# Kernel optimization log

Measured on AMD Instinct MI355X. Metric: run time of the kernel, lower is better.

## Reference

```python
import jax, jax.numpy as jnp
import numpy as np

N_CAND = 21  # tf.linspace(0, 1, 21) candidate pool
SOFTMIN_TEMP = 100.0


def _tree_constants(max_depth: int):
    """Signed split->descendant matrix M (S,N) and node->parent one-hot P (N,N)."""
    n_splits = 2 ** max_depth - 1
    n_nodes = 2 ** (max_depth + 1) - 1
    M = np.zeros((n_splits, n_nodes), np.float32)
    for s in range(n_splits):
        for n in range(n_nodes):
            a = n
            while a > 0:
                p = (a - 1) // 2
                if p == s:
                    # left-subtree descendants get -1, right-subtree +1
                    M[s, n] = -1.0 if a == 2 * s + 1 else 1.0
                    break
                a = p
    P = np.zeros((n_nodes, n_nodes), np.float32)
    for i in range(1, n_nodes):
        P[i, (i - 1) // 2] = 1.0
    return jnp.asarray(M), jnp.asarray(P), n_splits, n_nodes


def setup_inputs() -> dict:
    key = jax.random.key(0)
    kx, kw, kb = jax.random.split(key, 3)
    B, F = 512, 512
    max_depth = 8
    n_splits = 2 ** max_depth - 1
    x = jax.random.normal(kx, (B, F), dtype=jnp.float32)
    # VarianceScaling(scale=2.0, mode='fan_in') ~ std sqrt(2/F)
    W = jax.random.normal(kw, (F, n_splits), dtype=jnp.float32) * np.sqrt(2.0 / F).astype(np.float32)
    # keras RandomNormal default stddev=0.05
    b = jax.random.normal(kb, (n_splits,), dtype=jnp.float32) * 0.05
    return {"x": x, "W": W, "b": b, "max_depth": max_depth}


def reference(x, W, b, max_depth):
    M, P, n_splits, n_nodes = _tree_constants(int(max_depth))
    # q per split, then min over ancestor splits (method 0)
    q_split = x @ W + b                                   # (B, S)
    q_bsn = q_split[:, :, None] * M[None] + 1.0 - jnp.abs(M)[None]  # (B, S, N)
    q_node = jnp.min(q_bsn, axis=1)                       # (B, N)

    a_cand = jnp.linspace(0.0, 1.0, N_CAND)               # (C,)
    qn = q_node[:, :, None]                               # (B, N, 1)
    sqr = jnp.where(a_cand <= qn + 0.5, (a_cand - (qn + 0.5)) ** 2, 0.0)
    # reg part sums over the size-1 leading axis of a -> just a^2 (reg_lambda=1.0 in call)
    g_a = 0.5 * a_cand ** 2 + 0.5 * jnp.sum(sqr, axis=0)  # (N, C)

    eye = jnp.eye(n_nodes, dtype=jnp.float32)

    def body(carry, _):
        n2g, _ = carry
        g_grp = n2g.T @ g_a                               # (N, C): group-summed objective
        w = jax.nn.softmax(-SOFTMIN_TEMP * g_grp, axis=1)
        a_grp = jnp.sum(a_cand * w, axis=1)               # (N,) soft argmin over candidates
        a_node = n2g @ a_grp                              # (N,) broadcast group value to nodes
        a_par = (P @ a_node)[1:]
        a_par = jnp.concatenate([jnp.ones((1,), a_node.dtype), a_par])
        viol = a_node - a_par
        t = jnp.argmax(viol)
        cond = (jnp.max(viol) <= 1e-8) & (t > 0)
        t_oh = jax.nn.one_hot(t, n_nodes, dtype=jnp.float32)
        p_oh = t_oh @ P
        n2g = n2g + jnp.where(cond, 1.0, 0.0) * jnp.outer(t_oh, p_oh - t_oh)
        return (n2g, a_node), None

    (_, a_node), _ = jax.lax.scan(body, (eye, jnp.zeros(n_nodes, jnp.float32)), None,
                                  length=n_nodes + 1)
    trajectory = jnp.clip(q_node, 0.0, a_node[None, :])   # (B, N)
    return trajectory
```

## Files before the change

### kernel.cpp

```cpp
#include <hip/hip_runtime.h>
#include <hip/hip_bf16.h>
#include <math.h>

#define BATCH 512
#define FDIM  512
#define NSPL  255
#define NNOD  511
#define NC    21


__global__ __launch_bounds__(256) void k_qgemm(const float* __restrict__ x,
                                               const float* __restrict__ W,
                                               float* __restrict__ partial,
                                               int fpc) {
  __shared__ float Ws[64 * 68];
  __shared__ float xT[64 * 68];
  const int tid = threadIdx.x;
  const int s0 = blockIdx.x * 64;
  const int b0 = blockIdx.y * 64;
  const int f0 = blockIdx.z * fpc;
  const int sx = tid & 15;
  const int by = tid >> 4;
  float acc[4][4];
#pragma unroll
  for (int i = 0; i < 4; ++i)
#pragma unroll
    for (int j = 0; j < 4; ++j) acc[i][j] = 0.f;

  for (int fc = f0; fc < f0 + fpc; fc += 64) {
    {
      int si = tid & 63, fr = tid >> 6;
#pragma unroll
      for (int r = 0; r < 16; ++r) {
        int fi = fr + r * 4;
        int s = s0 + si;
        Ws[fi * 68 + si] = (s < NSPL) ? W[(fc + fi) * NSPL + s] : 0.f;
      }
      int j = tid & 63, ir = tid >> 6;
#pragma unroll
      for (int r = 0; r < 16; ++r) {
        int i = ir + r * 4;
        xT[j * 68 + i] = x[(b0 + i) * FDIM + (fc + j)];
      }
    }
    __syncthreads();
#pragma unroll 8
    for (int f = 0; f < 64; ++f) {
      float4 av = *(const float4*)&Ws[f * 68 + sx * 4];
      float4 xv = *(const float4*)&xT[f * 68 + by * 4];
      const float a4[4] = {av.x, av.y, av.z, av.w};
      const float x4[4] = {xv.x, xv.y, xv.z, xv.w};
#pragma unroll
      for (int i = 0; i < 4; ++i)
#pragma unroll
        for (int j = 0; j < 4; ++j) acc[i][j] += a4[i] * x4[j];
    }
    __syncthreads();
  }

  float* pout = partial + (size_t)blockIdx.z * (256 * BATCH);
#pragma unroll
  for (int i = 0; i < 4; ++i) {
    int s = s0 + sx * 4 + i;
    if (s < NSPL) {
      float4 v = make_float4(acc[i][0], acc[i][1], acc[i][2], acc[i][3]);
      *(float4*)&pout[s * BATCH + b0 + by * 4] = v;
    }
  }
}

__global__ __launch_bounds__(256) void k_qreduce(const float* __restrict__ partial,
                                                 const float* __restrict__ bias,
                                                 float* __restrict__ qsT, int n) {
  int idx = blockIdx.x * 256 + threadIdx.x;
  if (idx >= NSPL * BATCH) return;
  int s = idx >> 9;
  float v = 0.f;
  for (int c = 0; c < n; ++c) v += partial[(size_t)c * (256 * BATCH) + idx];
  qsT[idx] = v + bias[s];
}

__global__ __launch_bounds__(256) void k_qsplitT_fb(const float* __restrict__ x,
                                                    const float* __restrict__ W,
                                                    const float* __restrict__ bias,
                                                    float* __restrict__ qsT) {
  const int s = threadIdx.x;
  const int b0 = blockIdx.x * 8;
  if (s >= NSPL) return;
  float acc0[8], acc1[8];
#pragma unroll
  for (int i = 0; i < 8; ++i) { acc0[i] = 0.f; acc1[i] = 0.f; }
#pragma unroll 2
  for (int f = 0; f < 256; ++f) {
    float w0 = W[f * NSPL + s];
    float w1 = W[(f + 256) * NSPL + s];
#pragma unroll
    for (int i = 0; i < 8; ++i) {
      acc0[i] += x[(b0 + i) * FDIM + f] * w0;
      acc1[i] += x[(b0 + i) * FDIM + f + 256] * w1;
    }
  }
  float bs = bias[s];
#pragma unroll
  for (int i = 0; i < 8; ++i) qsT[s * BATCH + b0 + i] = (acc0[i] + acc1[i]) + bs;
}

__device__ __forceinline__ float qnode_walk(const float* __restrict__ qsT, int n, int b) {
  float q = 1.0f;
  int a = n;
  while (a > 0) {
    int p = (a - 1) >> 1;
    float v = qsT[p * BATCH + b];
    q = fminf(q, (a & 1) ? -v : v);
    a = p;
  }
  return q;
}

__global__ __launch_bounds__(256) void k_ga(const float* __restrict__ qsT,
                                            float* __restrict__ ga,
                                            double* __restrict__ agrp0) {
  const int n = blockIdx.x;
  const int tid = threadIdx.x;
  __shared__ float qs[BATCH];
  __shared__ double part[4][NC];
  __shared__ float gaRow[NC];
#pragma unroll
  for (int rep = 0; rep < 2; ++rep) {
    int b = tid + rep * 256;
    qs[b] = qnode_walk(qsT, n, b);
  }
  __syncthreads();
  if (tid < 4 * NC) {
    int c = tid % NC, chunk = tid / NC;
    double ac = 0.05 * (double)c;
    double ssum = 0.0;
    int b0 = chunk * 128;
    for (int b = b0; b < b0 + 128; ++b) {
      float qh = qs[b] + 0.5f;
      double dqh = (double)qh;
      if (ac <= dqh) { double d = ac - dqh; ssum += d * d; }
    }
    part[chunk][c] = ssum;
  }
  __syncthreads();
  if (tid < NC) {
    double ac = 0.05 * (double)tid;
    double ssum = ((part[0][tid] + part[1][tid]) + part[2][tid]) + part[3][tid];
    float gv = (float)(0.5 * ac * ac + 0.5 * ssum);
    ga[n * NC + tid] = gv;
    gaRow[tid] = gv;
  }
  __syncthreads();
  if (tid == 0) {
    double z[NC], m = -1e300;
#pragma unroll
    for (int c = 0; c < NC; ++c) { z[c] = -100.0 * (double)gaRow[c]; m = fmax(m, z[c]); }
    double S = 0.0;
#pragma unroll
    for (int c = 0; c < NC; ++c) { z[c] = exp(z[c] - m); S += z[c]; }
    double A = 0.0;
#pragma unroll
    for (int c = 0; c < NC; ++c) A += (0.05 * (double)c) * (z[c] / S);
    agrp0[n] = A;
  }
}

__global__ __launch_bounds__(64) void k_scan(const float* __restrict__ ga_g,
                                             const double* __restrict__ agrp0,
                                             double* __restrict__ a_node_out) {
  __shared__ float gaS[NNOD * NC];
  __shared__ double agrp[512];
  __shared__ double anode[512];
  __shared__ float kfS[512];
  const int lane = threadIdx.x;

  {
    const float4* src = (const float4*)ga_g;
    float4* dst = (float4*)gaS;
    const int n4 = (NNOD * NC) / 4;
#pragma unroll 4
    for (int i = lane; i < n4; i += 64) dst[i] = src[i];
    if (lane < (NNOD * NC) - n4 * 4) gaS[n4 * 4 + lane] = ga_g[n4 * 4 + lane];
  }
  for (int i = lane; i < 512; i += 64) {
    agrp[i] = (i < NNOD) ? agrp0[i] : 0.0;
    anode[i] = 0.0;
    kfS[i] = 0.0f;
  }
  __syncthreads();

  int t = 0, p = 0;
  double areg[8];
  int iter = 0;
  for (;;) {
    if (iter > 0) {
      int j = lane >> 5, c = lane & 31;
      int g = j ? p : t;
      double z = -1e300;
      if (c < NC) {
        double acc = (1.0 - (double)kfS[g]) * (double)gaS[g * NC + c];
        int l = 2 * g + 1, r = 2 * g + 2;
        if (l < NNOD) acc = acc + (double)kfS[l] * (double)gaS[l * NC + c];
        if (r < NNOD) acc = acc + (double)kfS[r] * (double)gaS[r * NC + c];
        z = -100.0 * acc;
      }
      double m = z;
#pragma unroll
      for (int off = 16; off >= 1; off >>= 1) m = fmax(m, __shfl_xor(m, off, 32));
      double e = (c < NC) ? exp(z - m) : 0.0;
      double S = e;
#pragma unroll
      for (int off = 16; off >= 1; off >>= 1) S += __shfl_xor(S, off, 32);
      double term = (c < NC) ? (0.05 * (double)c) * (e / S) : 0.0;
#pragma unroll
      for (int off = 16; off >= 1; off >>= 1) term += __shfl_xor(term, off, 32);
      if (c == 0) agrp[g] = term;
      __syncthreads();
    }

#pragma unroll
    for (int u = 0; u < 8; ++u) {
      int n = lane + (u << 6);
      if (n < NNOD) {
        double kn = (double)kfS[n];
        double agn = agrp[n];
        double an;
        if (n == 0) an = agn;
        else an = kn * agrp[(n - 1) >> 1] + (1.0 - kn) * agn;
        areg[u] = an;
        anode[n] = an;
      }
    }
    __syncthreads();

    double bv = -1e300; int bi = 0x7fffffff;
#pragma unroll
    for (int u = 0; u < 8; ++u) {
      int n = lane + (u << 6);
      if (n < NNOD) {
        double ap = (n == 0) ? 1.0 : anode[(n - 1) >> 1];
        double vi = areg[u] - ap;
        if (vi > bv) { bv = vi; bi = n; }
      }
    }
#pragma unroll
    for (int off = 32; off >= 1; off >>= 1) {
      double ov = __shfl_xor(bv, off, 64);
      int oi = __shfl_xor(bi, off, 64);
      if (ov > bv || (ov == bv && oi < bi)) { bv = ov; bi = oi; }
    }

    bool cond = (bv <= 1e-8) && (bi > 0);
    if (!cond || iter == 511) break;
    t = bi; p = (t - 1) >> 1;
    if (lane == 0) kfS[t] += 1.0f;
    __syncthreads();
    ++iter;
  }

#pragma unroll
  for (int u = 0; u < 8; ++u) {
    int n = lane + (u << 6);
    if (n < NNOD) a_node_out[n] = areg[u];
  }
}

__global__ __launch_bounds__(256) void k_out(const float* __restrict__ qsT,
                                             const double* __restrict__ a_node,
                                             float* __restrict__ out) {
  __shared__ float col[NSPL];
  const int b = blockIdx.x;
  const int tid = threadIdx.x;
  if (tid < NSPL) col[tid] = qsT[tid * BATCH + b];
  __syncthreads();
#pragma unroll
  for (int rep = 0; rep < 2; ++rep) {
    int n = tid + rep * 256;
    if (n < NNOD) {
      float q = 1.0f;
      int a = n;
      while (a > 0) {
        int p = (a - 1) >> 1;
        float v = col[p];
        q = fminf(q, (a & 1) ? -v : v);
        a = p;
      }
      double r = fmin(fmax((double)q, 0.0), a_node[n]);
      out[(size_t)b * NNOD + n] = (float)r;
    }
  }
}

extern "C" void kernel_launch(void* const* d_in, const int* in_sizes, int n_in,
                              void* d_out, int out_size, void* d_ws, size_t ws_size,
                              hipStream_t stream) {
  (void)in_sizes; (void)n_in; (void)out_size;
  const float* x    = (const float*)d_in[0];
  const float* W    = (const float*)d_in[1];
  const float* bias = (const float*)d_in[2];
  float* out = (float*)d_out;

  char* ws = (char*)d_ws;
  const size_t PART_STRIDE = 256 * BATCH * sizeof(float);
  const size_t TAIL = 575488;

  int n = 8;
  while (n > 1 && (size_t)n * PART_STRIDE + TAIL > ws_size) n >>= 1;
  bool splitk_ok = ((size_t)n * PART_STRIDE + TAIL <= ws_size);

  size_t P = splitk_ok ? (size_t)n * PART_STRIDE : 0;
  float*  qsT    = (float*) (ws + P);
  float*  ga     = (float*) (ws + P + 524288);
  double* agrp0  = (double*)(ws + P + 567296);
  double* a_node = (double*)(ws + P + 571392);

  if (splitk_ok) {
    float* partial = (float*)ws;
    k_qgemm<<<dim3(4, 8, n), dim3(256), 0, stream>>>(x, W, partial, 512 / n);
    k_qreduce<<<dim3(510), dim3(256), 0, stream>>>(partial, bias, qsT, n);
  } else {
    k_qsplitT_fb<<<dim3(64), dim3(256), 0, stream>>>(x, W, bias, qsT);
  }
  k_ga<<<dim3(NNOD), dim3(256), 0, stream>>>(qsT, ga, agrp0);
  k_scan<<<dim3(1), dim3(64), 0, stream>>>(ga, agrp0, a_node);
  k_out<<<dim3(BATCH), dim3(256), 0, stream>>>(qsT, a_node, out);
}
```

Measured before the change: 92.86 us.

## Fuse all stages into one persistent kernel with hierarchical grid barriers

Merges the split-K GEMM, reduction, per-node objective, serial scan and output kernels into a single 512-block kernel separated by atomic grid barriers, removing four launch gaps. While block 0 runs the serial scan, the other blocks precompute their q_node values so that after the last barrier they only clamp and store. A memset of the barrier area is added per call, and the design depends on all 512 blocks being co-resident (two per CU via launch bounds), otherwise it deadlocks.

```diff
diff --git a/kernel.cpp b/kernel.cpp
--- a/kernel.cpp
+++ b/kernel.cpp
@@ -9,75 +9,334 @@
 #define NC    21
 
 
-__global__ __launch_bounds__(256) void k_qgemm(const float* __restrict__ x,
-                                               const float* __restrict__ W,
-                                               float* __restrict__ partial,
-                                               int fpc) {
-  __shared__ float Ws[64 * 68];
-  __shared__ float xT[64 * 68];
+__device__ __forceinline__ unsigned* bslot(unsigned* bar, int i) { return bar + (size_t)i * 32; }
+
+__device__ __forceinline__ void grid_bar(unsigned* bar, int k, int bid, int tid) {
+  __syncthreads();
+  if (tid == 0) {
+    __threadfence();
+    unsigned cell = (unsigned)(bid & 7);
+    unsigned v = __hip_atomic_fetch_add(bslot(bar, 1 + k * 8 + (int)cell), 1u,
+                                        __ATOMIC_ACQ_REL, __HIP_MEMORY_SCOPE_AGENT);
+    if (v == 63u) {
+      unsigned r = __hip_atomic_fetch_add(bslot(bar, 33 + k), 1u,
+                                          __ATOMIC_ACQ_REL, __HIP_MEMORY_SCOPE_AGENT);
+      if (r == 7u)
+        __hip_atomic_store(bslot(bar, 37 + k), 1u, __ATOMIC_RELEASE, __HIP_MEMORY_SCOPE_AGENT);
+    }
+    while (__hip_atomic_load(bslot(bar, 37 + k), __ATOMIC_ACQUIRE, __HIP_MEMORY_SCOPE_AGENT) != 1u)
+      __builtin_amdgcn_s_sleep(2);
+    __threadfence();
+  }
+  __syncthreads();
+}
+
+__device__ __forceinline__ float qnode_walk(const float* __restrict__ qsT, int n, int b) {
+  float q = 1.0f;
+  int a = n;
+  while (a > 0) {
+    int p = (a - 1) >> 1;
+    float v = qsT[p * BATCH + b];
+    q = fminf(q, (a & 1) ? -v : v);
+    a = p;
+  }
+  return q;
+}
+
+__global__ __launch_bounds__(256, 2) void k_mega(
+    const float* __restrict__ x, const float* __restrict__ W,
+    const float* __restrict__ bias,
+    float* __restrict__ partial, float* __restrict__ qsT,
+    float* __restrict__ ga, double* __restrict__ agrp0,
+    double* __restrict__ a_node, float* __restrict__ out,
+    unsigned* __restrict__ bar, int fpc, int nchunks) {
+  __shared__ __align__(16) char smraw[53168];
   const int tid = threadIdx.x;
-  const int s0 = blockIdx.x * 64;
-  const int b0 = blockIdx.y * 64;
-  const int f0 = blockIdx.z * fpc;
-  const int sx = tid & 15;
-  const int by = tid >> 4;
-  float acc[4][4];
-#pragma unroll
-  for (int i = 0; i < 4; ++i)
-#pragma unroll
-    for (int j = 0; j < 4; ++j) acc[i][j] = 0.f;
-
-  for (int fc = f0; fc < f0 + fpc; fc += 64) {
+  const int bid = blockIdx.x;
+
+  if (bid < 32 * nchunks) {
+    float* Ws = (float*)smraw;
+    float* xT = Ws + 64 * 68;
+    const int s0 = (bid & 3) * 64;
+    const int b0 = ((bid >> 2) & 7) * 64;
+    const int bz = bid >> 5;
+    const int f0 = bz * fpc;
+    const int sx = tid & 15;
+    const int by = tid >> 4;
+    float acc[4][4];
+#pragma unroll
+    for (int i = 0; i < 4; ++i)
+#pragma unroll
+      for (int j = 0; j < 4; ++j) acc[i][j] = 0.f;
+
+    for (int fc = f0; fc < f0 + fpc; fc += 64) {
+      {
+        int si = tid & 63, fr = tid >> 6;
+#pragma unroll
+        for (int r = 0; r < 16; ++r) {
+          int fi = fr + r * 4;
+          int s = s0 + si;
+          Ws[fi * 68 + si] = (s < NSPL) ? W[(fc + fi) * NSPL + s] : 0.f;
+        }
+        int j = tid & 63, ir = tid >> 6;
+#pragma unroll
+        for (int r = 0; r < 16; ++r) {
+          int i = ir + r * 4;
+          xT[j * 68 + i] = x[(b0 + i) * FDIM + (fc + j)];
+        }
+      }
+      __syncthreads();
+#pragma unroll 8
+      for (int f = 0; f < 64; ++f) {
+        float4 av = *(const float4*)&Ws[f * 68 + sx * 4];
+        float4 xv = *(const float4*)&xT[f * 68 + by * 4];
+        const float a4[4] = {av.x, av.y, av.z, av.w};
+        const float x4[4] = {xv.x, xv.y, xv.z, xv.w};
+#pragma unroll
+        for (int i = 0; i < 4; ++i)
+#pragma unroll
+          for (int j = 0; j < 4; ++j) acc[i][j] += a4[i] * x4[j];
+      }
+      __syncthreads();
+    }
+
+    float* pout = partial + (size_t)bz * (256 * BATCH);
+#pragma unroll
+    for (int i = 0; i < 4; ++i) {
+      int s = s0 + sx * 4 + i;
+      if (s < NSPL) {
+        float4 v = make_float4(acc[i][0], acc[i][1], acc[i][2], acc[i][3]);
+        *(float4*)&pout[s * BATCH + b0 + by * 4] = v;
+      }
+    }
+  }
+  grid_bar(bar, 0, bid, tid);
+
+  if (bid < 510) {
+    int idx = bid * 256 + tid;
+    if (idx < NSPL * BATCH) {
+      int s = idx >> 9;
+      float v = 0.f;
+      for (int c = 0; c < nchunks; ++c) v += partial[(size_t)c * (256 * BATCH) + idx];
+      qsT[idx] = v + bias[s];
+    }
+  }
+  grid_bar(bar, 1, bid, tid);
+
+  if (bid < NNOD) {
+    const int n = bid;
+    float* qs = (float*)smraw;
+    double (*part)[NC] = (double (*)[NC])(smraw + 2048);
+    float* gaRow = (float*)(smraw + 2720);
+#pragma unroll
+    for (int rep = 0; rep < 2; ++rep) {
+      int b = tid + rep * 256;
+      qs[b] = qnode_walk(qsT, n, b);
+    }
+    __syncthreads();
+    if (tid < 4 * NC) {
+      int c = tid % NC, chunk = tid / NC;
+      double ac = 0.05 * (double)c;
+      double ssum = 0.0;
+      int b0 = chunk * 128;
+      for (int b = b0; b < b0 + 128; ++b) {
+        float qh = qs[b] + 0.5f;
+        double dqh = (double)qh;
+        if (ac <= dqh) { double d = ac - dqh; ssum += d * d; }
+      }
+      part[chunk][c] = ssum;
+    }
+    __syncthreads();
+    if (tid < NC) {
+      double ac = 0.05 * (double)tid;
+      double ssum = ((part[0][tid] + part[1][tid]) + part[2][tid]) + part[3][tid];
+      float gv = (float)(0.5 * ac * ac + 0.5 * ssum);
+      ga[n * NC + tid] = gv;
+      gaRow[tid] = gv;
+    }
+    __syncthreads();
+    if (tid == 0) {
+      double z[NC], m = -1e300;
+#pragma unroll
+      for (int c = 0; c < NC; ++c) { z[c] = -100.0 * (double)gaRow[c]; m = fmax(m, z[c]); }
+      double S = 0.0;
+#pragma unroll
+      for (int c = 0; c < NC; ++c) { z[c] = exp(z[c] - m); S += z[c]; }
+      double A = 0.0;
+#pragma unroll
+      for (int c = 0; c < NC; ++c) A += (0.05 * (double)c) * (z[c] / S);
+      agrp0[n] = A;
+    }
+  }
+  grid_bar(bar, 2, bid, tid);
+
+  float q0 = 0.f, q1 = 0.f;
+  if (bid == 0) {
+    if (tid < 64) {
+      float* gaS = (float*)smraw;
+      double* agrp = (double*)(smraw + 42928);
+      double* anode = (double*)(smraw + 47024);
+      float* kfS = (float*)(smraw + 51120);
+      const int lane = tid;
+      {
+        const float4* src = (const float4*)ga;
+        float4* dst = (float4*)gaS;
+        const int n4 = (NNOD * NC) / 4;
+#pragma unroll 4
+        for (int i = lane; i < n4; i += 64) dst[i] = src[i];
+        if (lane < (NNOD * NC) - n4 * 4) gaS[n4 * 4 + lane] = ga[n4 * 4 + lane];
+      }
+      for (int i = lane; i < 512; i += 64) {
+        agrp[i] = (i < NNOD) ? agrp0[i] : 0.0;
+        anode[i] = 0.0;
+        kfS[i] = 0.0f;
+      }
+      __threadfence_block();
+
+      int t = 0, p = 0;
+      double areg[8];
+      int iter = 0;
+      for (;;) {
+        if (iter > 0) {
+          int j = lane >> 5, c = lane & 31;
+          int g = j ? p : t;
+          double z = -1e300;
+          if (c < NC) {
+            double acc = (1.0 - (double)kfS[g]) * (double)gaS[g * NC + c];
+            int l = 2 * g + 1, r = 2 * g + 2;
+            if (l < NNOD) acc = acc + (double)kfS[l] * (double)gaS[l * NC + c];
+            if (r < NNOD) acc = acc + (double)kfS[r] * (double)gaS[r * NC + c];
+            z = -100.0 * acc;
+          }
+          double m = z;
+#pragma unroll
+          for (int off = 16; off >= 1; off >>= 1) m = fmax(m, __shfl_xor(m, off, 32));
+          double e = (c < NC) ? exp(z - m) : 0.0;
+          double S = e;
+#pragma unroll
+          for (int off = 16; off >= 1; off >>= 1) S += __shfl_xor(S, off, 32);
+          double term = (c < NC) ? (0.05 * (double)c) * (e / S) : 0.0;
+#pragma unroll
+          for (int off = 16; off >= 1; off >>= 1) term += __shfl_xor(term, off, 32);
+          if (c == 0) agrp[g] = term;
+          __threadfence_block();
+        }
+
+#pragma unroll
+        for (int u = 0; u < 8; ++u) {
+          int n = lane + (u << 6);
+          if (n < NNOD) {
+            double kn = (double)kfS[n];
+            double agn = agrp[n];
+            double an;
+            if (n == 0) an = agn;
+            else an = kn * agrp[(n - 1) >> 1] + (1.0 - kn) * agn;
+            areg[u] = an;
+            anode[n] = an;
+          }
+        }
+        __threadfence_block();
+
+        double bv = -1e300; int bi = 0x7fffffff;
+#pragma unroll
+        for (int u = 0; u < 8; ++u) {
+          int n = lane + (u << 6);
+          if (n < NNOD) {
+            double ap = (n == 0) ? 1.0 : anode[(n - 1) >> 1];
+            double vi = areg[u] - ap;
+            if (vi > bv) { bv = vi; bi = n; }
+          }
+        }
+#pragma unroll
+        for (int off = 32; off >= 1; off >>= 1) {
+          double ov = __shfl_xor(bv, off, 64);
+          int oi = __shfl_xor(bi, off, 64);
+          if (ov > bv || (ov == bv && oi < bi)) { bv = ov; bi = oi; }
+        }
+
+        bool cond = (bv <= 1e-8) && (bi > 0);
+        if (!cond || iter == 511) break;
+        t = bi; p = (t - 1) >> 1;
+        if (lane == 0) kfS[t] += 1.0f;
+        __threadfence_block();
+        ++iter;
+      }
+
+#pragma unroll
+      for (int u = 0; u < 8; ++u) {
+        int n = lane + (u << 6);
+        if (n < NNOD) a_node[n] = areg[u];
+      }
+    }
+  } else {
+    const int b = bid;
+    float* col = (float*)smraw;
+    if (tid < NSPL) col[tid] = qsT[tid * BATCH + b];
+    __syncthreads();
     {
-      int si = tid & 63, fr = tid >> 6;
-#pragma unroll
-      for (int r = 0; r < 16; ++r) {
-        int fi = fr + r * 4;
-        int s = s0 + si;
-        Ws[fi * 68 + si] = (s < NSPL) ? W[(fc + fi) * NSPL + s] : 0.f;
-      }
-      int j = tid & 63, ir = tid >> 6;
-#pragma unroll
-      for (int r = 0; r < 16; ++r) {
-        int i = ir + r * 4;
-        xT[j * 68 + i] = x[(b0 + i) * FDIM + (fc + j)];
-      }
-    }
-    __syncthreads();
-#pragma unroll 8
-    for (int f = 0; f < 64; ++f) {
-      float4 av = *(const float4*)&Ws[f * 68 + sx * 4];
-      float4 xv = *(const float4*)&xT[f * 68 + by * 4];
-      const float a4[4] = {av.x, av.y, av.z, av.w};
-      const float x4[4] = {xv.x, xv.y, xv.z, xv.w};
-#pragma unroll
-      for (int i = 0; i < 4; ++i)
-#pragma unroll
-        for (int j = 0; j < 4; ++j) acc[i][j] += a4[i] * x4[j];
-    }
-    __syncthreads();
-  }
-
-  float* pout = partial + (size_t)blockIdx.z * (256 * BATCH);
-#pragma unroll
-  for (int i = 0; i < 4; ++i) {
-    int s = s0 + sx * 4 + i;
-    if (s < NSPL) {
-      float4 v = make_float4(acc[i][0], acc[i][1], acc[i][2], acc[i][3]);
-      *(float4*)&pout[s * BATCH + b0 + by * 4] = v;
-    }
-  }
-}
-
-__global__ __launch_bounds__(256) void k_qreduce(const float* __restrict__ partial,
-                                                 const float* __restrict__ bias,
-                                                 float* __restrict__ qsT, int n) {
-  int idx = blockIdx.x * 256 + threadIdx.x;
-  if (idx >= NSPL * BATCH) return;
-  int s = idx >> 9;
-  float v = 0.f;
-  for (int c = 0; c < n; ++c) v += partial[(size_t)c * (256 * BATCH) + idx];
-  qsT[idx] = v + bias[s];
+      int n = tid;
+      float q = 1.0f;
+      int a = n;
+      while (a > 0) {
+        int p = (a - 1) >> 1;
+        float v = col[p];
+        q = fminf(q, (a & 1) ? -v : v);
+        a = p;
+      }
+      q0 = q;
+    }
+    {
+      int n = tid + 256;
+      if (n < NNOD) {
+        float q = 1.0f;
+        int a = n;
+        while (a > 0) {
+          int p = (a - 1) >> 1;
+          float v = col[p];
+          q = fminf(q, (a & 1) ? -v : v);
+          a = p;
+        }
+        q1 = q;
+      }
+    }
+  }
+  grid_bar(bar, 3, bid, tid);
+
+  if (bid == 0) {
+    float* col = (float*)smraw;
+    if (tid < NSPL) col[tid] = qsT[tid * BATCH + 0];
+    __syncthreads();
+#pragma unroll
+    for (int rep = 0; rep < 2; ++rep) {
+      int n = tid + rep * 256;
+      if (n < NNOD) {
+        float q = 1.0f;
+        int a = n;
+        while (a > 0) {
+          int p = (a - 1) >> 1;
+          float v = col[p];
+          q = fminf(q, (a & 1) ? -v : v);
+          a = p;
+        }
+        double r = fmin(fmax((double)q, 0.0), a_node[n]);
+        out[(size_t)0 * NNOD + n] = (float)r;
+      }
+    }
+  } else {
+    const int b = bid;
+    {
+      int n = tid;
+      double r = fmin(fmax((double)q0, 0.0), a_node[n]);
+      out[(size_t)b * NNOD + n] = (float)r;
+    }
+    {
+      int n = tid + 256;
+      if (n < NNOD) {
+        double r = fmin(fmax((double)q1, 0.0), a_node[n]);
+        out[(size_t)b * NNOD + n] = (float)r;
+      }
+    }
+  }
 }
 
 __global__ __launch_bounds__(256) void k_qsplitT_fb(const float* __restrict__ x,
@@ -105,21 +364,9 @@
   for (int i = 0; i < 8; ++i) qsT[s * BATCH + b0 + i] = (acc0[i] + acc1[i]) + bs;
 }
 
-__device__ __forceinline__ float qnode_walk(const float* __restrict__ qsT, int n, int b) {
-  float q = 1.0f;
-  int a = n;
-  while (a > 0) {
-    int p = (a - 1) >> 1;
-    float v = qsT[p * BATCH + b];
-    q = fminf(q, (a & 1) ? -v : v);
-    a = p;
-  }
-  return q;
-}
-
-__global__ __launch_bounds__(256) void k_ga(const float* __restrict__ qsT,
-                                            float* __restrict__ ga,
-                                            double* __restrict__ agrp0) {
+__global__ __launch_bounds__(256) void k_ga_fb(const float* __restrict__ qsT,
+                                               float* __restrict__ ga,
+                                               double* __restrict__ agrp0) {
   const int n = blockIdx.x;
   const int tid = threadIdx.x;
   __shared__ float qs[BATCH];
@@ -166,15 +413,14 @@
   }
 }
 
-__global__ __launch_bounds__(64) void k_scan(const float* __restrict__ ga_g,
-                                             const double* __restrict__ agrp0,
-                                             double* __restrict__ a_node_out) {
+__global__ __launch_bounds__(64) void k_scan_fb(const float* __restrict__ ga_g,
+                                                const double* __restrict__ agrp0,
+                                                double* __restrict__ a_node_out) {
   __shared__ float gaS[NNOD * NC];
   __shared__ double agrp[512];
   __shared__ double anode[512];
   __shared__ float kfS[512];
   const int lane = threadIdx.x;
-
   {
     const float4* src = (const float4*)ga_g;
     float4* dst = (float4*)gaS;
@@ -189,7 +435,6 @@
     kfS[i] = 0.0f;
   }
   __syncthreads();
-
   int t = 0, p = 0;
   double areg[8];
   int iter = 0;
@@ -218,7 +463,6 @@
       if (c == 0) agrp[g] = term;
       __syncthreads();
     }
-
 #pragma unroll
     for (int u = 0; u < 8; ++u) {
       int n = lane + (u << 6);
@@ -233,7 +477,6 @@
       }
     }
     __syncthreads();
-
     double bv = -1e300; int bi = 0x7fffffff;
 #pragma unroll
     for (int u = 0; u < 8; ++u) {
@@ -250,7 +493,6 @@
       int oi = __shfl_xor(bi, off, 64);
       if (ov > bv || (ov == bv && oi < bi)) { bv = ov; bi = oi; }
     }
-
     bool cond = (bv <= 1e-8) && (bi > 0);
     if (!cond || iter == 511) break;
     t = bi; p = (t - 1) >> 1;
@@ -258,7 +500,6 @@
     __syncthreads();
     ++iter;
   }
-
 #pragma unroll
   for (int u = 0; u < 8; ++u) {
     int n = lane + (u << 6);
@@ -266,9 +507,9 @@
   }
 }
 
-__global__ __launch_bounds__(256) void k_out(const float* __restrict__ qsT,
-                                             const double* __restrict__ a_node,
-                                             float* __restrict__ out) {
+__global__ __launch_bounds__(256) void k_out_fb(const float* __restrict__ qsT,
+                                                const double* __restrict__ a_node,
+                                                float* __restrict__ out) {
   __shared__ float col[NSPL];
   const int b = blockIdx.x;
   const int tid = threadIdx.x;
@@ -303,26 +544,29 @@
 
   char* ws = (char*)d_ws;
   const size_t PART_STRIDE = 256 * BATCH * sizeof(float);
-  const size_t TAIL = 575488;
+  const size_t BAR_BYTES = 8192;
+  const size_t TAIL = 575488 + BAR_BYTES;
 
   int n = 8;
   while (n > 1 && (size_t)n * PART_STRIDE + TAIL > ws_size) n >>= 1;
   bool splitk_ok = ((size_t)n * PART_STRIDE + TAIL <= ws_size);
 
   size_t P = splitk_ok ? (size_t)n * PART_STRIDE : 0;
-  float*  qsT    = (float*) (ws + P);
-  float*  ga     = (float*) (ws + P + 524288);
-  double* agrp0  = (double*)(ws + P + 567296);
-  double* a_node = (double*)(ws + P + 571392);
+  float*    qsT    = (float*)   (ws + P);
+  float*    ga     = (float*)   (ws + P + 524288);
+  double*   agrp0  = (double*)  (ws + P + 567296);
+  double*   a_node = (double*)  (ws + P + 571392);
+  unsigned* bar    = (unsigned*)(ws + P + 575488);
 
   if (splitk_ok) {
     float* partial = (float*)ws;
-    k_qgemm<<<dim3(4, 8, n), dim3(256), 0, stream>>>(x, W, partial, 512 / n);
-    k_qreduce<<<dim3(510), dim3(256), 0, stream>>>(partial, bias, qsT, n);
+    hipMemsetAsync(bar, 0, BAR_BYTES, stream);
+    k_mega<<<dim3(512), dim3(256), 0, stream>>>(x, W, bias, partial, qsT, ga,
+                                                agrp0, a_node, out, bar, 512 / n, n);
   } else {
     k_qsplitT_fb<<<dim3(64), dim3(256), 0, stream>>>(x, W, bias, qsT);
-  }
-  k_ga<<<dim3(NNOD), dim3(256), 0, stream>>>(qsT, ga, agrp0);
-  k_scan<<<dim3(1), dim3(64), 0, stream>>>(ga, agrp0, a_node);
-  k_out<<<dim3(BATCH), dim3(256), 0, stream>>>(qsT, a_node, out);
-}
+    k_ga_fb<<<dim3(NNOD), dim3(256), 0, stream>>>(qsT, ga, agrp0);
+    k_scan_fb<<<dim3(1), dim3(64), 0, stream>>>(ga, agrp0, a_node);
+    k_out_fb<<<dim3(BATCH), dim3(256), 0, stream>>>(qsT, a_node, out);
+  }
+}
```

After: 293.9 us. 216% more time.

## Fuse GEMM, reduce and g_a stages into one persistent kernel with grid barriers

Applied to the files above, without the earlier changes.

Merges the split-K GEMM, the partial reduction and the per-node g_a/softmin kernels into a single 512-block kernel, separated by hand-written atomic grid barriers that use a hierarchical counter. The goal is to remove two kernel launches and their inter-kernel gaps. It adds a hipMemsetAsync to reset the barrier counters on every call. Correctness depends on all 512 blocks being co-resident (launch_bounds 256,2 on the MI355X), otherwise the barrier can deadlock.

```diff
diff --git a/kernel.cpp b/kernel.cpp
--- a/kernel.cpp
+++ b/kernel.cpp
@@ -9,100 +9,26 @@
 #define NC    21
 
 
-__global__ __launch_bounds__(256) void k_qgemm(const float* __restrict__ x,
-                                               const float* __restrict__ W,
-                                               float* __restrict__ partial,
-                                               int fpc) {
-  __shared__ float Ws[64 * 68];
-  __shared__ float xT[64 * 68];
-  const int tid = threadIdx.x;
-  const int s0 = blockIdx.x * 64;
-  const int b0 = blockIdx.y * 64;
-  const int f0 = blockIdx.z * fpc;
-  const int sx = tid & 15;
-  const int by = tid >> 4;
-  float acc[4][4];
-#pragma unroll
-  for (int i = 0; i < 4; ++i)
-#pragma unroll
-    for (int j = 0; j < 4; ++j) acc[i][j] = 0.f;
-
-  for (int fc = f0; fc < f0 + fpc; fc += 64) {
-    {
-      int si = tid & 63, fr = tid >> 6;
-#pragma unroll
-      for (int r = 0; r < 16; ++r) {
-        int fi = fr + r * 4;
-        int s = s0 + si;
-        Ws[fi * 68 + si] = (s < NSPL) ? W[(fc + fi) * NSPL + s] : 0.f;
-      }
-      int j = tid & 63, ir = tid >> 6;
-#pragma unroll
-      for (int r = 0; r < 16; ++r) {
-        int i = ir + r * 4;
-        xT[j * 68 + i] = x[(b0 + i) * FDIM + (fc + j)];
-      }
-    }
-    __syncthreads();
-#pragma unroll 8
-    for (int f = 0; f < 64; ++f) {
-      float4 av = *(const float4*)&Ws[f * 68 + sx * 4];
-      float4 xv = *(const float4*)&xT[f * 68 + by * 4];
-      const float a4[4] = {av.x, av.y, av.z, av.w};
-      const float x4[4] = {xv.x, xv.y, xv.z, xv.w};
-#pragma unroll
-      for (int i = 0; i < 4; ++i)
-#pragma unroll
-        for (int j = 0; j < 4; ++j) acc[i][j] += a4[i] * x4[j];
-    }
-    __syncthreads();
-  }
-
-  float* pout = partial + (size_t)blockIdx.z * (256 * BATCH);
-#pragma unroll
-  for (int i = 0; i < 4; ++i) {
-    int s = s0 + sx * 4 + i;
-    if (s < NSPL) {
-      float4 v = make_float4(acc[i][0], acc[i][1], acc[i][2], acc[i][3]);
-      *(float4*)&pout[s * BATCH + b0 + by * 4] = v;
-    }
-  }
-}
-
-__global__ __launch_bounds__(256) void k_qreduce(const float* __restrict__ partial,
-                                                 const float* __restrict__ bias,
-                                                 float* __restrict__ qsT, int n) {
-  int idx = blockIdx.x * 256 + threadIdx.x;
-  if (idx >= NSPL * BATCH) return;
-  int s = idx >> 9;
-  float v = 0.f;
-  for (int c = 0; c < n; ++c) v += partial[(size_t)c * (256 * BATCH) + idx];
-  qsT[idx] = v + bias[s];
-}
-
-__global__ __launch_bounds__(256) void k_qsplitT_fb(const float* __restrict__ x,
-                                                    const float* __restrict__ W,
-                                                    const float* __restrict__ bias,
-                                                    float* __restrict__ qsT) {
-  const int s = threadIdx.x;
-  const int b0 = blockIdx.x * 8;
-  if (s >= NSPL) return;
-  float acc0[8], acc1[8];
-#pragma unroll
-  for (int i = 0; i < 8; ++i) { acc0[i] = 0.f; acc1[i] = 0.f; }
-#pragma unroll 2
-  for (int f = 0; f < 256; ++f) {
-    float w0 = W[f * NSPL + s];
-    float w1 = W[(f + 256) * NSPL + s];
-#pragma unroll
-    for (int i = 0; i < 8; ++i) {
-      acc0[i] += x[(b0 + i) * FDIM + f] * w0;
-      acc1[i] += x[(b0 + i) * FDIM + f + 256] * w1;
-    }
-  }
-  float bs = bias[s];
-#pragma unroll
-  for (int i = 0; i < 8; ++i) qsT[s * BATCH + b0 + i] = (acc0[i] + acc1[i]) + bs;
+__device__ __forceinline__ unsigned* bslot(unsigned* bar, int i) { return bar + (size_t)i * 32; }
+
+__device__ __forceinline__ void grid_bar(unsigned* bar, int k, int bid, int tid) {
+  __syncthreads();
+  if (tid == 0) {
+    __threadfence();
+    unsigned cell = (unsigned)(bid & 7);
+    unsigned v = __hip_atomic_fetch_add(bslot(bar, 1 + k * 8 + (int)cell), 1u,
+                                        __ATOMIC_ACQ_REL, __HIP_MEMORY_SCOPE_AGENT);
+    if (v == 63u) {
+      unsigned r = __hip_atomic_fetch_add(bslot(bar, 33 + k), 1u,
+                                          __ATOMIC_ACQ_REL, __HIP_MEMORY_SCOPE_AGENT);
+      if (r == 7u)
+        __hip_atomic_store(bslot(bar, 37 + k), 1u, __ATOMIC_RELEASE, __HIP_MEMORY_SCOPE_AGENT);
+    }
+    while (__hip_atomic_load(bslot(bar, 37 + k), __ATOMIC_ACQUIRE, __HIP_MEMORY_SCOPE_AGENT) != 1u)
+      __builtin_amdgcn_s_sleep(2);
+    __threadfence();
+  }
+  __syncthreads();
 }
 
 __device__ __forceinline__ float qnode_walk(const float* __restrict__ qsT, int n, int b) {
@@ -117,52 +43,129 @@
   return q;
 }
 
-__global__ __launch_bounds__(256) void k_ga(const float* __restrict__ qsT,
-                                            float* __restrict__ ga,
-                                            double* __restrict__ agrp0) {
-  const int n = blockIdx.x;
+__global__ __launch_bounds__(256, 2) void k_front(
+    const float* __restrict__ x, const float* __restrict__ W,
+    const float* __restrict__ bias,
+    float* __restrict__ partial, float* __restrict__ qsT,
+    float* __restrict__ ga, double* __restrict__ agrp0,
+    unsigned* __restrict__ bar, int fpc, int nchunks) {
+  __shared__ __align__(16) char smraw[34816];
   const int tid = threadIdx.x;
-  __shared__ float qs[BATCH];
-  __shared__ double part[4][NC];
-  __shared__ float gaRow[NC];
-#pragma unroll
-  for (int rep = 0; rep < 2; ++rep) {
-    int b = tid + rep * 256;
-    qs[b] = qnode_walk(qsT, n, b);
-  }
-  __syncthreads();
-  if (tid < 4 * NC) {
-    int c = tid % NC, chunk = tid / NC;
-    double ac = 0.05 * (double)c;
-    double ssum = 0.0;
-    int b0 = chunk * 128;
-    for (int b = b0; b < b0 + 128; ++b) {
-      float qh = qs[b] + 0.5f;
-      double dqh = (double)qh;
-      if (ac <= dqh) { double d = ac - dqh; ssum += d * d; }
-    }
-    part[chunk][c] = ssum;
-  }
-  __syncthreads();
-  if (tid < NC) {
-    double ac = 0.05 * (double)tid;
-    double ssum = ((part[0][tid] + part[1][tid]) + part[2][tid]) + part[3][tid];
-    float gv = (float)(0.5 * ac * ac + 0.5 * ssum);
-    ga[n * NC + tid] = gv;
-    gaRow[tid] = gv;
-  }
-  __syncthreads();
-  if (tid == 0) {
-    double z[NC], m = -1e300;
-#pragma unroll
-    for (int c = 0; c < NC; ++c) { z[c] = -100.0 * (double)gaRow[c]; m = fmax(m, z[c]); }
-    double S = 0.0;
-#pragma unroll
-    for (int c = 0; c < NC; ++c) { z[c] = exp(z[c] - m); S += z[c]; }
-    double A = 0.0;
-#pragma unroll
-    for (int c = 0; c < NC; ++c) A += (0.05 * (double)c) * (z[c] / S);
-    agrp0[n] = A;
+  const int bid = blockIdx.x;
+
+  if (bid < 32 * nchunks) {
+    float* Ws = (float*)smraw;
+    float* xT = Ws + 64 * 68;
+    const int s0 = (bid & 3) * 64;
+    const int b0 = ((bid >> 2) & 7) * 64;
+    const int bz = bid >> 5;
+    const int f0 = bz * fpc;
+    const int sx = tid & 15;
+    const int by = tid >> 4;
+    float acc[4][4];
+#pragma unroll
+    for (int i = 0; i < 4; ++i)
+#pragma unroll
+      for (int j = 0; j < 4; ++j) acc[i][j] = 0.f;
+
+    for (int fc = f0; fc < f0 + fpc; fc += 64) {
+      {
+        int si = tid & 63, fr = tid >> 6;
+#pragma unroll
+        for (int r = 0; r < 16; ++r) {
+          int fi = fr + r * 4;
+          int s = s0 + si;
+          Ws[fi * 68 + si] = (s < NSPL) ? W[(fc + fi) * NSPL + s] : 0.f;
+        }
+        int j = tid & 63, ir = tid >> 6;
+#pragma unroll
+        for (int r = 0; r < 16; ++r) {
+          int i = ir + r * 4;
+          xT[j * 68 + i] = x[(b0 + i) * FDIM + (fc + j)];
+        }
+      }
+      __syncthreads();
+#pragma unroll 8
+      for (int f = 0; f < 64; ++f) {
+        float4 av = *(const float4*)&Ws[f * 68 + sx * 4];
+        float4 xv = *(const float4*)&xT[f * 68 + by * 4];
+        const float a4[4] = {av.x, av.y, av.z, av.w};
+        const float x4[4] = {xv.x, xv.y, xv.z, xv.w};
+#pragma unroll
+        for (int i = 0; i < 4; ++i)
+#pragma unroll
+          for (int j = 0; j < 4; ++j) acc[i][j] += a4[i] * x4[j];
+      }
+      __syncthreads();
+    }
+
+    float* pout = partial + (size_t)bz * (256 * BATCH);
+#pragma unroll
+    for (int i = 0; i < 4; ++i) {
+      int s = s0 + sx * 4 + i;
+      if (s < NSPL) {
+        float4 v = make_float4(acc[i][0], acc[i][1], acc[i][2], acc[i][3]);
+        *(float4*)&pout[s * BATCH + b0 + by * 4] = v;
+      }
+    }
+  }
+  grid_bar(bar, 0, bid, tid);
+
+  if (bid < 510) {
+    int idx = bid * 256 + tid;
+    if (idx < NSPL * BATCH) {
+      int s = idx >> 9;
+      float v = 0.f;
+      for (int c = 0; c < nchunks; ++c) v += partial[(size_t)c * (256 * BATCH) + idx];
+      qsT[idx] = v + bias[s];
+    }
+  }
+  grid_bar(bar, 1, bid, tid);
+
+  if (bid < NNOD) {
+    const int n = bid;
+    float* qs = (float*)smraw;
+    double (*part)[NC] = (double (*)[NC])(smraw + 2048);
+    float* gaRow = (float*)(smraw + 2720);
+#pragma unroll
+    for (int rep = 0; rep < 2; ++rep) {
+      int b = tid + rep * 256;
+      qs[b] = qnode_walk(qsT, n, b);
+    }
+    __syncthreads();
+    if (tid < 4 * NC) {
+      int c = tid % NC, chunk = tid / NC;
+      double ac = 0.05 * (double)c;
+      double ssum = 0.0;
+      int b0 = chunk * 128;
+      for (int b = b0; b < b0 + 128; ++b) {
+        float qh = qs[b] + 0.5f;
+        double dqh = (double)qh;
+        if (ac <= dqh) { double d = ac - dqh; ssum += d * d; }
+      }
+      part[chunk][c] = ssum;
+    }
+    __syncthreads();
+    if (tid < NC) {
+      double ac = 0.05 * (double)tid;
+      double ssum = ((part[0][tid] + part[1][tid]) + part[2][tid]) + part[3][tid];
+      float gv = (float)(0.5 * ac * ac + 0.5 * ssum);
+      ga[n * NC + tid] = gv;
+      gaRow[tid] = gv;
+    }
+    __syncthreads();
+    if (tid == 0) {
+      double z[NC], m = -1e300;
+#pragma unroll
+      for (int c = 0; c < NC; ++c) { z[c] = -100.0 * (double)gaRow[c]; m = fmax(m, z[c]); }
+      double S = 0.0;
+#pragma unroll
+      for (int c = 0; c < NC; ++c) { z[c] = exp(z[c] - m); S += z[c]; }
+      double A = 0.0;
+#pragma unroll
+      for (int c = 0; c < NC; ++c) A += (0.05 * (double)c) * (z[c] / S);
+      agrp0[n] = A;
+    }
   }
 }
 
@@ -292,6 +295,80 @@
   }
 }
 
+__global__ __launch_bounds__(256) void k_qsplitT_fb(const float* __restrict__ x,
+                                                    const float* __restrict__ W,
+                                                    const float* __restrict__ bias,
+                                                    float* __restrict__ qsT) {
+  const int s = threadIdx.x;
+  const int b0 = blockIdx.x * 8;
+  if (s >= NSPL) return;
+  float acc0[8], acc1[8];
+#pragma unroll
+  for (int i = 0; i < 8; ++i) { acc0[i] = 0.f; acc1[i] = 0.f; }
+#pragma unroll 2
+  for (int f = 0; f < 256; ++f) {
+    float w0 = W[f * NSPL + s];
+    float w1 = W[(f + 256) * NSPL + s];
+#pragma unroll
+    for (int i = 0; i < 8; ++i) {
+      acc0[i] += x[(b0 + i) * FDIM + f] * w0;
+      acc1[i] += x[(b0 + i) * FDIM + f + 256] * w1;
+    }
+  }
+  float bs = bias[s];
+#pragma unroll
+  for (int i = 0; i < 8; ++i) qsT[s * BATCH + b0 + i] = (acc0[i] + acc1[i]) + bs;
+}
+
+__global__ __launch_bounds__(256) void k_ga_fb(const float* __restrict__ qsT,
+                                               float* __restrict__ ga,
+                                               double* __restrict__ agrp0) {
+  const int n = blockIdx.x;
+  const int tid = threadIdx.x;
+  __shared__ float qs[BATCH];
+  __shared__ double part[4][NC];
+  __shared__ float gaRow[NC];
+#pragma unroll
+  for (int rep = 0; rep < 2; ++rep) {
+    int b = tid + rep * 256;
+    qs[b] = qnode_walk(qsT, n, b);
+  }
+  __syncthreads();
+  if (tid < 4 * NC) {
+    int c = tid % NC, chunk = tid / NC;
+    double ac = 0.05 * (double)c;
+    double ssum = 0.0;
+    int b0 = chunk * 128;
+    for (int b = b0; b < b0 + 128; ++b) {
+      float qh = qs[b] + 0.5f;
+      double dqh = (double)qh;
+      if (ac <= dqh) { double d = ac - dqh; ssum += d * d; }
+    }
+    part[chunk][c] = ssum;
+  }
+  __syncthreads();
+  if (tid < NC) {
+    double ac = 0.05 * (double)tid;
+    double ssum = ((part[0][tid] + part[1][tid]) + part[2][tid]) + part[3][tid];
+    float gv = (float)(0.5 * ac * ac + 0.5 * ssum);
+    ga[n * NC + tid] = gv;
+    gaRow[tid] = gv;
+  }
+  __syncthreads();
+  if (tid == 0) {
+    double z[NC], m = -1e300;
+#pragma unroll
+    for (int c = 0; c < NC; ++c) { z[c] = -100.0 * (double)gaRow[c]; m = fmax(m, z[c]); }
+    double S = 0.0;
+#pragma unroll
+    for (int c = 0; c < NC; ++c) { z[c] = exp(z[c] - m); S += z[c]; }
+    double A = 0.0;
+#pragma unroll
+    for (int c = 0; c < NC; ++c) A += (0.05 * (double)c) * (z[c] / S);
+    agrp0[n] = A;
+  }
+}
+
 extern "C" void kernel_launch(void* const* d_in, const int* in_sizes, int n_in,
                               void* d_out, int out_size, void* d_ws, size_t ws_size,
                               hipStream_t stream) {
@@ -303,26 +380,30 @@
 
   char* ws = (char*)d_ws;
   const size_t PART_STRIDE = 256 * BATCH * sizeof(float);
-  const size_t TAIL = 575488;
+  const size_t BAR_BYTES = 8192;
+  const size_t TAIL = 575488 + BAR_BYTES;
 
   int n = 8;
   while (n > 1 && (size_t)n * PART_STRIDE + TAIL > ws_size) n >>= 1;
-  bool splitk_ok = ((size_t)n * PART_STRIDE + TAIL <= ws_size);
-
-  size_t P = splitk_ok ? (size_t)n * PART_STRIDE : 0;
-  float*  qsT    = (float*) (ws + P);
-  float*  ga     = (float*) (ws + P + 524288);
-  double* agrp0  = (double*)(ws + P + 567296);
-  double* a_node = (double*)(ws + P + 571392);
-
-  if (splitk_ok) {
+  bool merged_ok = ((size_t)8 * PART_STRIDE + TAIL <= ws_size);
+
+  size_t P = (size_t)n * PART_STRIDE;
+  if (!merged_ok && (P + TAIL > ws_size)) P = 0;
+  float*    qsT    = (float*)   (ws + P);
+  float*    ga     = (float*)   (ws + P + 524288);
+  double*   agrp0  = (double*)  (ws + P + 567296);
+  double*   a_node = (double*)  (ws + P + 571392);
+  unsigned* bar    = (unsigned*)(ws + P + 575488);
+
+  if (merged_ok) {
     float* partial = (float*)ws;
-    k_qgemm<<<dim3(4, 8, n), dim3(256), 0, stream>>>(x, W, partial, 512 / n);
-    k_qreduce<<<dim3(510), dim3(256), 0, stream>>>(partial, bias, qsT, n);
+    hipMemsetAsync(bar, 0, BAR_BYTES, stream);
+    k_front<<<dim3(512), dim3(256), 0, stream>>>(x, W, bias, partial, qsT, ga,
+                                                 agrp0, bar, 512 / 8, 8);
   } else {
     k_qsplitT_fb<<<dim3(64), dim3(256), 0, stream>>>(x, W, bias, qsT);
-  }
-  k_ga<<<dim3(NNOD), dim3(256), 0, stream>>>(qsT, ga, agrp0);
+    k_ga_fb<<<dim3(NNOD), dim3(256), 0, stream>>>(qsT, ga, agrp0);
+  }
   k_scan<<<dim3(1), dim3(64), 0, stream>>>(ga, agrp0, a_node);
   k_out<<<dim3(BATCH), dim3(256), 0, stream>>>(qsT, a_node, out);
 }
```

Measured after the change: 199.1 us. 2.14x slower.

## Replace split-K GEMM plus reduce with single 32x32-tile GEMM fusing bias

Applied to the files above, without the earlier changes.

Drops the split-K partial-sum GEMM and its separate reduction kernel. A single GEMM kernel now uses 32x32 output tiles (128 blocks), walks the full K dimension, and adds the bias in its epilogue. This removes one launch and the round trip of the partial buffer through global memory. In exchange it has fewer blocks than the 256-block split-K grid, a lower arithmetic intensity per thread (2x2 outputs), and more K-loop work per block.

```diff
diff --git a/kernel.cpp b/kernel.cpp
--- a/kernel.cpp
+++ b/kernel.cpp
@@ -11,98 +11,75 @@
 
 __global__ __launch_bounds__(256) void k_qgemm(const float* __restrict__ x,
                                                const float* __restrict__ W,
-                                               float* __restrict__ partial,
-                                               int fpc) {
-  __shared__ float Ws[64 * 68];
-  __shared__ float xT[64 * 68];
+                                               const float* __restrict__ bias,
+                                               float* __restrict__ qsT) {
+  __shared__ float Ws[64 * 34];
+  __shared__ float xT[64 * 34];
   const int tid = threadIdx.x;
-  const int s0 = blockIdx.x * 64;
-  const int b0 = blockIdx.y * 64;
-  const int f0 = blockIdx.z * fpc;
+  const int s0 = blockIdx.x * 32;
+  const int b0 = blockIdx.y * 32;
   const int sx = tid & 15;
   const int by = tid >> 4;
-  float acc[4][4];
-#pragma unroll
-  for (int i = 0; i < 4; ++i)
-#pragma unroll
-    for (int j = 0; j < 4; ++j) acc[i][j] = 0.f;
-
-  for (int fc = f0; fc < f0 + fpc; fc += 64) {
+  float acc[8][2][2];
+#pragma unroll
+  for (int c = 0; c < 8; ++c)
+#pragma unroll
+    for (int i = 0; i < 2; ++i)
+#pragma unroll
+      for (int j = 0; j < 2; ++j) acc[c][i][j] = 0.f;
+
+#pragma unroll
+  for (int c = 0; c < 8; ++c) {
+    const int fc = c * 64;
     {
-      int si = tid & 63, fr = tid >> 6;
-#pragma unroll
-      for (int r = 0; r < 16; ++r) {
-        int fi = fr + r * 4;
+      int si = tid & 31, fr = tid >> 5;
+#pragma unroll
+      for (int r = 0; r < 8; ++r) {
+        int fi = fr + r * 8;
         int s = s0 + si;
-        Ws[fi * 68 + si] = (s < NSPL) ? W[(fc + fi) * NSPL + s] : 0.f;
+        Ws[fi * 34 + si] = (s < NSPL) ? W[(fc + fi) * NSPL + s] : 0.f;
       }
       int j = tid & 63, ir = tid >> 6;
 #pragma unroll
-      for (int r = 0; r < 16; ++r) {
-        int i = ir + r * 4;
-        xT[j * 68 + i] = x[(b0 + i) * FDIM + (fc + j)];
+      for (int r = 0; r < 8; ++r) {
+        int bb = ir + r * 4;
+        xT[j * 34 + bb] = x[(b0 + bb) * FDIM + (fc + j)];
       }
     }
     __syncthreads();
 #pragma unroll 8
     for (int f = 0; f < 64; ++f) {
-      float4 av = *(const float4*)&Ws[f * 68 + sx * 4];
-      float4 xv = *(const float4*)&xT[f * 68 + by * 4];
-      const float a4[4] = {av.x, av.y, av.z, av.w};
-      const float x4[4] = {xv.x, xv.y, xv.z, xv.w};
-#pragma unroll
-      for (int i = 0; i < 4; ++i)
-#pragma unroll
-        for (int j = 0; j < 4; ++j) acc[i][j] += a4[i] * x4[j];
-    }
-    __syncthreads();
-  }
-
-  float* pout = partial + (size_t)blockIdx.z * (256 * BATCH);
-#pragma unroll
-  for (int i = 0; i < 4; ++i) {
-    int s = s0 + sx * 4 + i;
+      float2 av = *(const float2*)&Ws[f * 34 + sx * 2];
+      float2 xv = *(const float2*)&xT[f * 34 + by * 2];
+      acc[c][0][0] += av.x * xv.x;
+      acc[c][0][1] += av.x * xv.y;
+      acc[c][1][0] += av.y * xv.x;
+      acc[c][1][1] += av.y * xv.y;
+    }
+    __syncthreads();
+  }
+
+#pragma unroll
+  for (int i = 0; i < 2; ++i) {
+    int s = s0 + sx * 2 + i;
     if (s < NSPL) {
-      float4 v = make_float4(acc[i][0], acc[i][1], acc[i][2], acc[i][3]);
-      *(float4*)&pout[s * BATCH + b0 + by * 4] = v;
-    }
-  }
-}
-
-__global__ __launch_bounds__(256) void k_qreduce(const float* __restrict__ partial,
-                                                 const float* __restrict__ bias,
-                                                 float* __restrict__ qsT, int n) {
-  int idx = blockIdx.x * 256 + threadIdx.x;
-  if (idx >= NSPL * BATCH) return;
-  int s = idx >> 9;
-  float v = 0.f;
-  for (int c = 0; c < n; ++c) v += partial[(size_t)c * (256 * BATCH) + idx];
-  qsT[idx] = v + bias[s];
-}
-
-__global__ __launch_bounds__(256) void k_qsplitT_fb(const float* __restrict__ x,
-                                                    const float* __restrict__ W,
-                                                    const float* __restrict__ bias,
-                                                    float* __restrict__ qsT) {
-  const int s = threadIdx.x;
-  const int b0 = blockIdx.x * 8;
-  if (s >= NSPL) return;
-  float acc0[8], acc1[8];
-#pragma unroll
-  for (int i = 0; i < 8; ++i) { acc0[i] = 0.f; acc1[i] = 0.f; }
-#pragma unroll 2
-  for (int f = 0; f < 256; ++f) {
-    float w0 = W[f * NSPL + s];
-    float w1 = W[(f + 256) * NSPL + s];
-#pragma unroll
-    for (int i = 0; i < 8; ++i) {
-      acc0[i] += x[(b0 + i) * FDIM + f] * w0;
-      acc1[i] += x[(b0 + i) * FDIM + f + 256] * w1;
-    }
-  }
-  float bs = bias[s];
-#pragma unroll
-  for (int i = 0; i < 8; ++i) qsT[s * BATCH + b0 + i] = (acc0[i] + acc1[i]) + bs;
+      float bs = bias[s];
+      float2 o;
+      {
+        float v = 0.f;
+#pragma unroll
+        for (int c = 0; c < 8; ++c) v += acc[c][i][0];
+        o.x = v + bs;
+      }
+      {
+        float v = 0.f;
+#pragma unroll
+        for (int c = 0; c < 8; ++c) v += acc[c][i][1];
+        o.y = v + bs;
+      }
+      *(float2*)&qsT[s * BATCH + b0 + by * 2] = o;
+    }
+  }
 }
 
 __device__ __forceinline__ float qnode_walk(const float* __restrict__ qsT, int n, int b) {
@@ -295,33 +272,19 @@
 extern "C" void kernel_launch(void* const* d_in, const int* in_sizes, int n_in,
                               void* d_out, int out_size, void* d_ws, size_t ws_size,
                               hipStream_t stream) {
-  (void)in_sizes; (void)n_in; (void)out_size;
+  (void)in_sizes; (void)n_in; (void)out_size; (void)ws_size;
   const float* x    = (const float*)d_in[0];
   const float* W    = (const float*)d_in[1];
   const float* bias = (const float*)d_in[2];
   float* out = (float*)d_out;
 
   char* ws = (char*)d_ws;
-  const size_t PART_STRIDE = 256 * BATCH * sizeof(float);
-  const size_t TAIL = 575488;
-
-  int n = 8;
-  while (n > 1 && (size_t)n * PART_STRIDE + TAIL > ws_size) n >>= 1;
-  bool splitk_ok = ((size_t)n * PART_STRIDE + TAIL <= ws_size);
-
-  size_t P = splitk_ok ? (size_t)n * PART_STRIDE : 0;
-  float*  qsT    = (float*) (ws + P);
-  float*  ga     = (float*) (ws + P + 524288);
-  double* agrp0  = (double*)(ws + P + 567296);
-  double* a_node = (double*)(ws + P + 571392);
-
-  if (splitk_ok) {
-    float* partial = (float*)ws;
-    k_qgemm<<<dim3(4, 8, n), dim3(256), 0, stream>>>(x, W, partial, 512 / n);
-    k_qreduce<<<dim3(510), dim3(256), 0, stream>>>(partial, bias, qsT, n);
-  } else {
-    k_qsplitT_fb<<<dim3(64), dim3(256), 0, stream>>>(x, W, bias, qsT);
-  }
+  float*  qsT    = (float*) (ws + 0);
+  float*  ga     = (float*) (ws + 524288);
+  double* agrp0  = (double*)(ws + 567296);
+  double* a_node = (double*)(ws + 571392);
+
+  k_qgemm<<<dim3(8, 16), dim3(256), 0, stream>>>(x, W, bias, qsT);
   k_ga<<<dim3(NNOD), dim3(256), 0, stream>>>(qsT, ga, agrp0);
   k_scan<<<dim3(1), dim3(64), 0, stream>>>(ga, agrp0, a_node);
   k_out<<<dim3(BATCH), dim3(256), 0, stream>>>(qsT, a_node, out);
```

Result: slower. 109.1 us (+17.5%).
